# Kernel tuning notes

Measured on AMD Instinct MI355X. Metric: run time of the kernel, lower is better.

## Reference

```python
import jax, jax.numpy as jnp
import numpy as np

B, F, T, D, O = 8192, 512, 64, 6, 128
N_INTERNAL = 2 ** D - 1  # 63
N_LEAVES = 2 ** D        # 64


def smooth_step(t):
    tc = jnp.clip(t, -0.5, 0.5)
    return -2.0 * tc ** 3 + 1.5 * tc + 0.5


def setup_inputs() -> dict:
    key = jax.random.key(0)
    k1, k2, k3, k4 = jax.random.split(key, 4)
    x = jax.random.normal(k1, (B, F), dtype=jnp.float32)
    # Stacked per-node Linear weights in BFS (heap) order: node i -> row i.
    W_nodes = jax.random.normal(k2, (N_INTERNAL, F, T), dtype=jnp.float32) * (1.0 / np.sqrt(F))
    b_nodes = jax.random.normal(k3, (N_INTERNAL, T), dtype=jnp.float32) * 0.01
    # Per-leaf mixing weight [out_features, num_trees], leaves in BFS order.
    W_leaf = jax.random.normal(k4, (N_LEAVES, O, T), dtype=jnp.float32)
    return {"x": x, "W_nodes": W_nodes, "b_nodes": b_nodes, "W_leaf": W_leaf}


def reference(x, W_nodes, b_nodes, W_leaf):
    n_internal = W_nodes.shape[0]
    depth = int(np.log2(n_internal + 1))
    # All internal-node gates in one stacked GEMM: [B, n_internal, T]
    s = smooth_step(jnp.einsum('bf,nft->bnt', x, W_nodes) + b_nodes[None, :, :])
    b, _, t = s.shape
    prob = jnp.ones((b, 1, t), dtype=s.dtype)  # root prob
    start = 0
    for lvl in range(depth):
        width = 2 ** lvl
        s_l = s[:, start:start + width]  # [B, width, T], nodes at this level
        start += width
        # node local j -> children local 2j (left, prob*s) and 2j+1 (right, prob*(1-s))
        prob = jnp.stack([prob * s_l, prob * (1.0 - s_l)], axis=2).reshape(b, 2 * width, t)
    # prob: [B, n_leaves, T]; mix per-leaf, per-tree weights -> [B, O]
    out = jnp.einsum('blt,lot->bo', prob, W_leaf)
    return out
```

## Files before the change

kernel.cpp:

```cpp
#include <hip/hip_runtime.h>
#include <hip/hip_fp16.h>

#define BATCH 8192
#define FDIM  512
#define NTREE 64
#define NODES 63
#define ODIM  128
#define NJP   4096
#define K2    4096
#define TPG   8

typedef _Float16 f16;
typedef _Float16 f16x2 __attribute__((ext_vector_type(2)));
typedef _Float16 f16x4 __attribute__((ext_vector_type(4)));
typedef _Float16 f16x8 __attribute__((ext_vector_type(8)));
typedef float    f32x4 __attribute__((ext_vector_type(4)));

#define XH_OFF   0
#define XH_SZ    ((size_t)BATCH*FDIM*2)
#define WNH_OFF  (XH_OFF + XH_SZ)
#define WNH_SZ   ((size_t)NJP*FDIM*2)
#define WLT_OFF  (WNH_OFF + WNH_SZ)
#define WLT_SZ   ((size_t)ODIM*K2*2)
#define PS_OFF   (WLT_OFF + WLT_SZ)
#define PS_SZ    ((size_t)TPG*BATCH*ODIM*4)
#define WS_NEEDED (PS_OFF + PS_SZ)

__device__ __forceinline__ float smooth_step_f(float t) {
    float tc = fminf(fmaxf(t, -0.5f), 0.5f);
    return fmaf(tc, fmaf(-2.0f * tc, tc, 1.5f), 0.5f);
}

__device__ __forceinline__ void async16(const void* g, void* l) {
    __builtin_amdgcn_global_load_lds((__attribute__((address_space(1))) void*)g,
                                     (__attribute__((address_space(3))) void*)l,
                                     16, 0, 0);
}

__device__ __forceinline__ int sw_off(int row, int g) {
    return ((row >> 3) * 512) + (((row & 7) * 8 + (g ^ (row & 7))) * 8);
}

#define XBLK 4096
#define WLBLK 128
__global__ __launch_bounds__(256)
void prep_kernel(const float* __restrict__ x, const float* __restrict__ wn,
                 const float* __restrict__ wl,
                 f16* __restrict__ xh, f16* __restrict__ wnh, f16* __restrict__ wlt)
{
    __shared__ __align__(16) char smem[16640];
    const int bid = blockIdx.x;

    if (bid < XBLK) {
        size_t i = ((size_t)bid * 256 + threadIdx.x) * 4;
        float4 v = *(const float4*)(x + i);
        f16x4 o4 = { (f16)v.x, (f16)v.y, (f16)v.z, (f16)v.w };
        *(f16x4*)(xh + i) = o4;
        return;
    }
    if (bid < XBLK + WLBLK) {
        f16 (*tile)[72] = (f16(*)[72])smem;
        const int o    = bid - XBLK;
        const int lane = threadIdx.x & 63;
        const int w    = threadIdx.x >> 6;
        #pragma unroll
        for (int lc = 0; lc < 16; ++lc) {
            int l = w * 16 + lc;
            tile[lane][l] = (f16)wl[(size_t)l * (ODIM * NTREE) + o * 64 + lane];
        }
        __syncthreads();
        f16* orow = wlt + (size_t)o * K2;
        #pragma unroll
        for (int c = 0; c < 2; ++c) {
            int idx = (threadIdx.x * 2 + c) * 8;
            int t = idx >> 6, l = idx & 63;
            f16x8 v;
            #pragma unroll
            for (int e = 0; e < 8; ++e) v[e] = tile[t][l + e];
            *(f16x8*)(orow + idx) = v;
        }
        return;
    }
    {
        const int id   = bid - (XBLK + WLBLK);
        const int n    = id & 63;
        const int f0   = (id >> 6) * 64;
        const int lane = threadIdx.x & 63;
        const int w    = threadIdx.x >> 6;
        if (n == NODES) {
            #pragma unroll
            for (int tc = 0; tc < 16; ++tc) {
                int t = w * 16 + tc;
                wnh[(size_t)(t * 64 + NODES) * FDIM + f0 + lane] = (f16)0.0f;
            }
            return;
        }
        float (*tile)[65] = (float(*)[65])smem;
        const float* src = wn + (size_t)n * (FDIM * NTREE);
        #pragma unroll
        for (int i = 0; i < 16; ++i) {
            int fl = w * 16 + i;
            tile[fl][lane] = src[(size_t)(f0 + fl) * NTREE + lane];
        }
        __syncthreads();
        #pragma unroll
        for (int i = 0; i < 16; ++i) {
            int t = w * 16 + i;
            wnh[(size_t)(t * 64 + n) * FDIM + f0 + lane] = (f16)tile[lane][t];
        }
    }
}

__global__ __launch_bounds__(256, 2)
void fused_tree(const f16* __restrict__ xh, const f16* __restrict__ wnh,
                const float* __restrict__ bn, const f16* __restrict__ wlt,
                float* __restrict__ partial)
{
    __shared__ f16 SH[16640];
    const int tid  = threadIdx.x;
    const int lane = tid & 63;
    const int w    = tid >> 6;
    const int wm   = w & 1;
    const int wn   = w >> 1;
    const int row0 = blockIdx.x * 128;
    const int tpg  = blockIdx.y;

    const int lr = lane >> 3;
    const int lg = (lane & 7) ^ lr;
    const int frow = tid & 127;
    const int ftr  = tid >> 7;

    f32x4 lacc[4][4] = {};

    for (int tpi = 0; tpi < 4; ++tpi) {
        const int tp = tpg * 4 + tpi;
        const int j0 = tp * 128;

        f32x4 acc[4][4] = {};
        for (int k0 = 0; k0 < FDIM; k0 += 64) {
            #pragma unroll
            for (int q = 0; q < 8; ++q) {
                int id = w * 8 + q;
                if (id < 16) {
                    int r = id * 8 + lr;
                    async16(xh + (size_t)(row0 + r) * FDIM + k0 + lg * 8, &SH[id * 512 + lane * 8]);
                } else {
                    int c = id - 16;
                    int r = c * 8 + lr;
                    async16(wnh + (size_t)(j0 + r) * FDIM + k0 + lg * 8, &SH[8192 + c * 512 + lane * 8]);
                }
            }
            __syncthreads();
            #pragma unroll
            for (int ks = 0; ks < 2; ++ks) {
                int g = ks * 4 + (lane >> 4);
                f16x8 bfr[4];
                #pragma unroll
                for (int tn = 0; tn < 4; ++tn) {
                    int j = wn * 64 + tn * 16 + (lane & 15);
                    bfr[tn] = *(const f16x8*)&SH[8192 + sw_off(j, g)];
                }
                #pragma unroll
                for (int tm = 0; tm < 4; ++tm) {
                    int m = wm * 64 + tm * 16 + (lane & 15);
                    f16x8 afr = *(const f16x8*)&SH[sw_off(m, g)];
                    #pragma unroll
                    for (int tn = 0; tn < 4; ++tn)
                        acc[tm][tn] = __builtin_amdgcn_mfma_f32_16x16x32_f16(afr, bfr[tn], acc[tm][tn], 0, 0, 0);
                }
            }
            __syncthreads();
        }

        #pragma unroll
        for (int tn = 0; tn < 4; ++tn) {
            int col = wn * 64 + tn * 16 + (lane & 15);
            int nn  = col & 63;
            int tt  = (j0 + col) >> 6;
            float bias = (nn < NODES) ? bn[nn * NTREE + tt] : 0.0f;
            #pragma unroll
            for (int tm = 0; tm < 4; ++tm) {
                #pragma unroll
                for (int r = 0; r < 4; ++r) {
                    int row = wm * 64 + tm * 16 + (lane >> 4) * 4 + r;
                    SH[row * 130 + col] = (f16)smooth_step_f(acc[tm][tn][r] + bias);
                }
            }
        }
        __syncthreads();

        f16x8 ov[8];
        {
            const f16* gp = &SH[frow * 130 + ftr * 64];
            float g[64];
            #pragma unroll
            for (int c = 0; c < 32; ++c) {
                f16x2 v = *(const f16x2*)(gp + 2 * c);
                g[2 * c]     = (float)v[0];
                g[2 * c + 1] = (float)v[1];
            }
            float pr[32];
            pr[0] = 1.0f;
            int bse = 0;
            #pragma unroll
            for (int lvl = 0; lvl < 5; ++lvl) {
                const int width = 1 << lvl;
                #pragma unroll
                for (int i = width - 1; i >= 0; --i) {
                    float p = pr[i], s = g[bse + i];
                    pr[2 * i]     = p * s;
                    pr[2 * i + 1] = p * (1.0f - s);
                }
                bse += width;
            }
            #pragma unroll
            for (int i = 0; i < 32; ++i) {
                float s5 = g[31 + i];
                float p  = pr[i];
                ov[i >> 2][(i & 3) * 2]     = (f16)(p * s5);
                ov[i >> 2][(i & 3) * 2 + 1] = (f16)(p * (1.0f - s5));
            }
        }
        __syncthreads();

        #pragma unroll
        for (int h = 0; h < 2; ++h) {
            if (ftr == h) {
                #pragma unroll
                for (int g2 = 0; g2 < 8; ++g2)
                    *(f16x8*)&SH[sw_off(frow, g2)] = ov[g2];
            }
            #pragma unroll
            for (int q = 0; q < 4; ++q) {
                int c = w * 4 + q;
                int o = c * 8 + lr;
                async16(wlt + (size_t)o * K2 + j0 + h * 64 + lg * 8,
                        &SH[8192 + c * 512 + lane * 8]);
            }
            __syncthreads();

            #pragma unroll
            for (int ks = 0; ks < 2; ++ks) {
                int g = ks * 4 + (lane >> 4);
                f16x8 bfr[4];
                #pragma unroll
                for (int tn = 0; tn < 4; ++tn) {
                    int o = wn * 64 + tn * 16 + (lane & 15);
                    bfr[tn] = *(const f16x8*)&SH[8192 + sw_off(o, g)];
                }
                #pragma unroll
                for (int tm = 0; tm < 4; ++tm) {
                    int m = wm * 64 + tm * 16 + (lane & 15);
                    f16x8 afr = *(const f16x8*)&SH[sw_off(m, g)];
                    #pragma unroll
                    for (int tn = 0; tn < 4; ++tn)
                        lacc[tm][tn] = __builtin_amdgcn_mfma_f32_16x16x32_f16(afr, bfr[tn], lacc[tm][tn], 0, 0, 0);
                }
            }
            __syncthreads();
        }
    }

    float* dst = partial + (size_t)tpg * BATCH * ODIM;
    #pragma unroll
    for (int tn = 0; tn < 4; ++tn) {
        int o = wn * 64 + tn * 16 + (lane & 15);
        #pragma unroll
        for (int tm = 0; tm < 4; ++tm) {
            #pragma unroll
            for (int r = 0; r < 4; ++r) {
                int row = row0 + wm * 64 + tm * 16 + (lane >> 4) * 4 + r;
                dst[(size_t)row * ODIM + o] = lacc[tm][tn][r];
            }
        }
    }
}

__global__ void reduce_kernel(const float* __restrict__ partial, float* __restrict__ out) {
    size_t i = ((size_t)blockIdx.x * blockDim.x + threadIdx.x) * 4;
    f32x4 a = *(const f32x4*)(partial + i);
    #pragma unroll
    for (int k = 1; k < TPG; ++k)
        a += *(const f32x4*)(partial + (size_t)k * BATCH * ODIM + i);
    *(f32x4*)(out + i) = a;
}

#define ROWS 8
__global__ __launch_bounds__(256, 2)
void soft_tree_fallback(const float* __restrict__ x, const float* __restrict__ Wn,
                        const float* __restrict__ bn, const float* __restrict__ Wl,
                        float* __restrict__ out)
{
    __shared__ __half s_lds[ROWS][NODES][NTREE];
    const int lane = threadIdx.x & 63;
    const int w    = threadIdx.x >> 6;
    const long row0 = (long)blockIdx.x * ROWS;
    for (int n = w; n < NODES; n += 4) {
        const float* wp = Wn + ((long)n * FDIM) * NTREE + lane;
        const float* xp = x + row0 * FDIM;
        float acc[ROWS];
        #pragma unroll
        for (int r = 0; r < ROWS; ++r) acc[r] = 0.0f;
        #pragma unroll 8
        for (int f = 0; f < FDIM; ++f) {
            float wv = wp[(long)f * NTREE];
            #pragma unroll
            for (int r = 0; r < ROWS; ++r)
                acc[r] = fmaf(xp[r * FDIM + f], wv, acc[r]);
        }
        float bias = bn[n * NTREE + lane];
        #pragma unroll
        for (int r = 0; r < ROWS; ++r)
            s_lds[r][n][lane] = __float2half(smooth_step_f(acc[r] + bias));
    }
    __syncthreads();
    const int r0 = w * 2, r1 = w * 2 + 1;
    float pr0[64], pr1[64];
    {
        pr0[0] = 1.0f; pr1[0] = 1.0f;
        int base = 0;
        #pragma unroll
        for (int lvl = 0; lvl < 6; ++lvl) {
            const int width = 1 << lvl;
            #pragma unroll
            for (int i = width - 1; i >= 0; --i) {
                float sa = __half2float(s_lds[r0][base + i][lane]);
                float sb = __half2float(s_lds[r1][base + i][lane]);
                float pa = pr0[i], pb = pr1[i];
                pr0[2 * i] = pa * sa; pr0[2 * i + 1] = pa * (1.0f - sa);
                pr1[2 * i] = pb * sb; pr1[2 * i + 1] = pb * (1.0f - sb);
            }
            base += width;
        }
    }
    for (int o = 0; o < ODIM; ++o) {
        const float* wlp = Wl + (long)o * NTREE + lane;
        float c0 = 0.0f, c1 = 0.0f;
        #pragma unroll
        for (int l = 0; l < 64; ++l) {
            float wv = wlp[(long)l * (ODIM * NTREE)];
            c0 = fmaf(pr0[l], wv, c0);
            c1 = fmaf(pr1[l], wv, c1);
        }
        #pragma unroll
        for (int off = 32; off > 0; off >>= 1) {
            c0 += __shfl_xor(c0, off, 64);
            c1 += __shfl_xor(c1, off, 64);
        }
        if (lane == 0) {
            out[(row0 + r0) * ODIM + o] = c0;
            out[(row0 + r1) * ODIM + o] = c1;
        }
    }
}

extern "C" void kernel_launch(void* const* d_in, const int* in_sizes, int n_in,
                              void* d_out, int out_size, void* d_ws, size_t ws_size,
                              hipStream_t stream) {
    const float* x  = (const float*)d_in[0];
    const float* Wn = (const float*)d_in[1];
    const float* bn = (const float*)d_in[2];
    const float* Wl = (const float*)d_in[3];
    float* out = (float*)d_out;

    if (ws_size < WS_NEEDED) {
        soft_tree_fallback<<<BATCH / ROWS, 256, 0, stream>>>(x, Wn, bn, Wl, out);
        return;
    }

    f16*   xh  = (f16*)((char*)d_ws + XH_OFF);
    f16*   wnh = (f16*)((char*)d_ws + WNH_OFF);
    f16*   wlt = (f16*)((char*)d_ws + WLT_OFF);
    float* ps  = (float*)((char*)d_ws + PS_OFF);

    prep_kernel<<<XBLK + WLBLK + 512, 256, 0, stream>>>(x, Wn, Wl, xh, wnh, wlt);
    fused_tree<<<dim3(BATCH / 128, TPG), 256, 0, stream>>>(xh, wnh, bn, wlt, ps);
    reduce_kernel<<<(BATCH * ODIM) / (256 * 4), 256, 0, stream>>>(ps, out);
}
```

Measured before the change: 149.7 us.

## Double-buffer node GEMM tiles and prefetch leaf weights during gate epilogue

Doubles LDS so the next k-slice of x and node weights loads asynchronously while MFMAs run on the current slice, leaving one barrier per k-step. Both halves of the leaf weight tile are prefetched into a separate LDS region before the smooth-step and tree-probability epilogue, so that load overlaps the epilogue. Both probability halves are stored at once, and some barriers become lighter LDS-only waits. The cost is about twice the LDS per block, which may limit occupancy.

Result: no change. 151.9 us (+1.5%).

```diff
diff --git a/kernel.cpp b/kernel.cpp
--- a/kernel.cpp
+++ b/kernel.cpp
@@ -37,6 +37,12 @@
                                      16, 0, 0);
 }
 
+__device__ __forceinline__ void bar_lds() {
+    asm volatile("s_waitcnt lgkmcnt(0)" ::: "memory");
+    __builtin_amdgcn_s_barrier();
+    asm volatile("" ::: "memory");
+}
+
 __device__ __forceinline__ int sw_off(int row, int g) {
     return ((row >> 3) * 512) + (((row & 7) * 8 + (g ^ (row & 7))) * 8);
 }
@@ -111,12 +117,30 @@
     }
 }
 
+#define STAGE_NODE(dstbase, kk)                                                \
+    {                                                                          \
+        _Pragma("unroll")                                                      \
+        for (int q = 0; q < 8; ++q) {                                          \
+            int id = w * 8 + q;                                                \
+            if (id < 16) {                                                     \
+                int r = id * 8 + lr;                                           \
+                async16(xh + (size_t)(row0 + r) * FDIM + (kk) + lg * 8,        \
+                        &SH[(dstbase) + id * 512 + lane * 8]);                 \
+            } else {                                                           \
+                int c = id - 16;                                               \
+                int r = c * 8 + lr;                                            \
+                async16(wnh + (size_t)(j0 + r) * FDIM + (kk) + lg * 8,         \
+                        &SH[(dstbase) + 8192 + c * 512 + lane * 8]);           \
+            }                                                                  \
+        }                                                                      \
+    }
+
 __global__ __launch_bounds__(256, 2)
 void fused_tree(const f16* __restrict__ xh, const f16* __restrict__ wnh,
                 const float* __restrict__ bn, const f16* __restrict__ wlt,
                 float* __restrict__ partial)
 {
-    __shared__ f16 SH[16640];
+    __shared__ __align__(16) f16 SH[33024];
     const int tid  = threadIdx.x;
     const int lane = tid & 63;
     const int w    = tid >> 6;
@@ -137,20 +161,14 @@
         const int j0 = tp * 128;
 
         f32x4 acc[4][4] = {};
-        for (int k0 = 0; k0 < FDIM; k0 += 64) {
-            #pragma unroll
-            for (int q = 0; q < 8; ++q) {
-                int id = w * 8 + q;
-                if (id < 16) {
-                    int r = id * 8 + lr;
-                    async16(xh + (size_t)(row0 + r) * FDIM + k0 + lg * 8, &SH[id * 512 + lane * 8]);
-                } else {
-                    int c = id - 16;
-                    int r = c * 8 + lr;
-                    async16(wnh + (size_t)(j0 + r) * FDIM + k0 + lg * 8, &SH[8192 + c * 512 + lane * 8]);
-                }
-            }
-            __syncthreads();
+        STAGE_NODE(0, 0);
+        __syncthreads();
+
+        #pragma unroll 2
+        for (int t = 0; t < 8; ++t) {
+            const int base = (t & 1) * 16384;
+            if (t < 7)
+                STAGE_NODE(((t + 1) & 1) * 16384, (t + 1) * 64);
             #pragma unroll
             for (int ks = 0; ks < 2; ++ks) {
                 int g = ks * 4 + (lane >> 4);
@@ -158,18 +176,28 @@
                 #pragma unroll
                 for (int tn = 0; tn < 4; ++tn) {
                     int j = wn * 64 + tn * 16 + (lane & 15);
-                    bfr[tn] = *(const f16x8*)&SH[8192 + sw_off(j, g)];
+                    bfr[tn] = *(const f16x8*)&SH[base + 8192 + sw_off(j, g)];
                 }
                 #pragma unroll
                 for (int tm = 0; tm < 4; ++tm) {
                     int m = wm * 64 + tm * 16 + (lane & 15);
-                    f16x8 afr = *(const f16x8*)&SH[sw_off(m, g)];
+                    f16x8 afr = *(const f16x8*)&SH[base + sw_off(m, g)];
                     #pragma unroll
                     for (int tn = 0; tn < 4; ++tn)
                         acc[tm][tn] = __builtin_amdgcn_mfma_f32_16x16x32_f16(afr, bfr[tn], acc[tm][tn], 0, 0, 0);
                 }
             }
             __syncthreads();
+        }
+
+        #pragma unroll
+        for (int q = 0; q < 8; ++q) {
+            int id = w * 8 + q;
+            int h  = id >> 4;
+            int c  = id & 15;
+            int o  = c * 8 + lr;
+            async16(wlt + (size_t)o * K2 + j0 + h * 64 + lg * 8,
+                    &SH[16640 + h * 8192 + c * 512 + lane * 8]);
         }
 
         #pragma unroll
@@ -187,18 +215,19 @@
                 }
             }
         }
-        __syncthreads();
+        bar_lds();
 
         f16x8 ov[8];
         {
             const f16* gp = &SH[frow * 130 + ftr * 64];
-            float g[64];
+            float gg[64];
             #pragma unroll
             for (int c = 0; c < 32; ++c) {
                 f16x2 v = *(const f16x2*)(gp + 2 * c);
-                g[2 * c]     = (float)v[0];
-                g[2 * c + 1] = (float)v[1];
-            }
+                gg[2 * c]     = (float)v[0];
+                gg[2 * c + 1] = (float)v[1];
+            }
+            bar_lds();
             float pr[32];
             pr[0] = 1.0f;
             int bse = 0;
@@ -207,7 +236,7 @@
                 const int width = 1 << lvl;
                 #pragma unroll
                 for (int i = width - 1; i >= 0; --i) {
-                    float p = pr[i], s = g[bse + i];
+                    float p = pr[i], s = gg[bse + i];
                     pr[2 * i]     = p * s;
                     pr[2 * i + 1] = p * (1.0f - s);
                 }
@@ -215,30 +244,20 @@
             }
             #pragma unroll
             for (int i = 0; i < 32; ++i) {
-                float s5 = g[31 + i];
+                float s5 = gg[31 + i];
                 float p  = pr[i];
                 ov[i >> 2][(i & 3) * 2]     = (f16)(p * s5);
                 ov[i >> 2][(i & 3) * 2 + 1] = (f16)(p * (1.0f - s5));
             }
         }
+
+        #pragma unroll
+        for (int g2 = 0; g2 < 8; ++g2)
+            *(f16x8*)&SH[ftr * 8192 + sw_off(frow, g2)] = ov[g2];
         __syncthreads();
 
         #pragma unroll
         for (int h = 0; h < 2; ++h) {
-            if (ftr == h) {
-                #pragma unroll
-                for (int g2 = 0; g2 < 8; ++g2)
-                    *(f16x8*)&SH[sw_off(frow, g2)] = ov[g2];
-            }
-            #pragma unroll
-            for (int q = 0; q < 4; ++q) {
-                int c = w * 4 + q;
-                int o = c * 8 + lr;
-                async16(wlt + (size_t)o * K2 + j0 + h * 64 + lg * 8,
-                        &SH[8192 + c * 512 + lane * 8]);
-            }
-            __syncthreads();
-
             #pragma unroll
             for (int ks = 0; ks < 2; ++ks) {
                 int g = ks * 4 + (lane >> 4);
@@ -246,19 +265,19 @@
                 #pragma unroll
                 for (int tn = 0; tn < 4; ++tn) {
                     int o = wn * 64 + tn * 16 + (lane & 15);
-                    bfr[tn] = *(const f16x8*)&SH[8192 + sw_off(o, g)];
+                    bfr[tn] = *(const f16x8*)&SH[16640 + h * 8192 + sw_off(o, g)];
                 }
                 #pragma unroll
                 for (int tm = 0; tm < 4; ++tm) {
                     int m = wm * 64 + tm * 16 + (lane & 15);
-                    f16x8 afr = *(const f16x8*)&SH[sw_off(m, g)];
+                    f16x8 afr = *(const f16x8*)&SH[h * 8192 + sw_off(m, g)];
                     #pragma unroll
                     for (int tn = 0; tn < 4; ++tn)
                         lacc[tm][tn] = __builtin_amdgcn_mfma_f32_16x16x32_f16(afr, bfr[tn], lacc[tm][tn], 0, 0, 0);
                 }
             }
-            __syncthreads();
-        }
+        }
+        __syncthreads();
     }
 
     float* dst = partial + (size_t)tpg * BATCH * ODIM;
```

## Pre-pack operands in MFMA fragment order and load fragments directly from global

Applied to the files above, without the earlier changes.

The prep kernel now writes x, node weights and leaf weights as f16 tiles already laid out in MFMA fragment order. The fused kernel then reads A/B fragments straight from global memory into registers instead of staging them through LDS with async loads and barriers. Both halves of the leaf-probability tile are also written to LDS at once, which removes per-half barriers. The cost is that every wave now depends on global or L2 latency for each fragment with no LDS reuse across waves, and the prep kernel does strided, uncoalesced reads of the weights.

After: 161.8 us. +8.1%, slower.

```diff
diff --git a/kernel.cpp b/kernel.cpp
--- a/kernel.cpp
+++ b/kernel.cpp
@@ -31,104 +31,93 @@
     return fmaf(tc, fmaf(-2.0f * tc, tc, 1.5f), 0.5f);
 }
 
-__device__ __forceinline__ void async16(const void* g, void* l) {
-    __builtin_amdgcn_global_load_lds((__attribute__((address_space(1))) void*)g,
-                                     (__attribute__((address_space(3))) void*)l,
-                                     16, 0, 0);
-}
-
 __device__ __forceinline__ int sw_off(int row, int g) {
     return ((row >> 3) * 512) + (((row & 7) * 8 + (g ^ (row & 7))) * 8);
 }
 
-#define XBLK 4096
-#define WLBLK 128
 __global__ __launch_bounds__(256)
 void prep_kernel(const float* __restrict__ x, const float* __restrict__ wn,
                  const float* __restrict__ wl,
-                 f16* __restrict__ xh, f16* __restrict__ wnh, f16* __restrict__ wlt)
+                 f16* __restrict__ xf, f16* __restrict__ wnf, f16* __restrict__ wlf)
 {
-    __shared__ __align__(16) char smem[16640];
-    const int bid = blockIdx.x;
-
-    if (bid < XBLK) {
-        size_t i = ((size_t)bid * 256 + threadIdx.x) * 4;
-        float4 v = *(const float4*)(x + i);
-        f16x4 o4 = { (f16)v.x, (f16)v.y, (f16)v.z, (f16)v.w };
-        *(f16x4*)(xh + i) = o4;
-        return;
-    }
-    if (bid < XBLK + WLBLK) {
-        f16 (*tile)[72] = (f16(*)[72])smem;
-        const int o    = bid - XBLK;
-        const int lane = threadIdx.x & 63;
-        const int w    = threadIdx.x >> 6;
-        #pragma unroll
-        for (int lc = 0; lc < 16; ++lc) {
-            int l = w * 16 + lc;
-            tile[lane][l] = (f16)wl[(size_t)l * (ODIM * NTREE) + o * 64 + lane];
-        }
-        __syncthreads();
-        f16* orow = wlt + (size_t)o * K2;
-        #pragma unroll
-        for (int c = 0; c < 2; ++c) {
-            int idx = (threadIdx.x * 2 + c) * 8;
-            int t = idx >> 6, l = idx & 63;
+    const int bid = blockIdx.x, tid = threadIdx.x;
+    if (bid < 512) {
+        const int bx = bid >> 3, k0 = bid & 7;
+        f16* dst = xf + ((size_t)bx * 8192 + (size_t)k0 * 1024) * 8;
+        #pragma unroll
+        for (int c = 0; c < 4; ++c) {
+            int fid  = c * 256 + tid;
+            int lane = fid & 63, ks = (fid >> 6) & 1, tm = (fid >> 7) & 3, wm = (fid >> 9) & 1;
+            int row  = bx * 128 + wm * 64 + tm * 16 + (lane & 15);
+            int k    = k0 * 64 + (ks * 4 + (lane >> 4)) * 8;
+            const float* s = x + (size_t)row * FDIM + k;
+            float4 a = *(const float4*)s, b = *(const float4*)(s + 4);
+            f16x8 v = { (f16)a.x, (f16)a.y, (f16)a.z, (f16)a.w,
+                        (f16)b.x, (f16)b.y, (f16)b.z, (f16)b.w };
+            *(f16x8*)(dst + (size_t)fid * 8) = v;
+        }
+    } else if (bid < 768) {
+        const int id = bid - 512, tp = id >> 3, k0 = id & 7;
+        f16* dst = wnf + ((size_t)tp * 8192 + (size_t)k0 * 1024) * 8;
+        #pragma unroll
+        for (int c = 0; c < 4; ++c) {
+            int fid  = c * 256 + tid;
+            int lane = fid & 63, ks = (fid >> 6) & 1, tn = (fid >> 7) & 3, wq = (fid >> 9) & 1;
+            int col  = tp * 128 + wq * 64 + tn * 16 + (lane & 15);
+            int t    = col >> 6, n = col & 63;
+            int k    = k0 * 64 + (ks * 4 + (lane >> 4)) * 8;
             f16x8 v;
-            #pragma unroll
-            for (int e = 0; e < 8; ++e) v[e] = tile[t][l + e];
-            *(f16x8*)(orow + idx) = v;
-        }
-        return;
-    }
-    {
-        const int id   = bid - (XBLK + WLBLK);
-        const int n    = id & 63;
-        const int f0   = (id >> 6) * 64;
-        const int lane = threadIdx.x & 63;
-        const int w    = threadIdx.x >> 6;
-        if (n == NODES) {
-            #pragma unroll
-            for (int tc = 0; tc < 16; ++tc) {
-                int t = w * 16 + tc;
-                wnh[(size_t)(t * 64 + NODES) * FDIM + f0 + lane] = (f16)0.0f;
-            }
-            return;
-        }
-        float (*tile)[65] = (float(*)[65])smem;
-        const float* src = wn + (size_t)n * (FDIM * NTREE);
-        #pragma unroll
-        for (int i = 0; i < 16; ++i) {
-            int fl = w * 16 + i;
-            tile[fl][lane] = src[(size_t)(f0 + fl) * NTREE + lane];
-        }
-        __syncthreads();
-        #pragma unroll
-        for (int i = 0; i < 16; ++i) {
-            int t = w * 16 + i;
-            wnh[(size_t)(t * 64 + n) * FDIM + f0 + lane] = (f16)tile[lane][t];
+            if (n == NODES) {
+                #pragma unroll
+                for (int e = 0; e < 8; ++e) v[e] = (f16)0.0f;
+            } else {
+                const float* s = wn + ((size_t)n * FDIM + k) * NTREE + t;
+                #pragma unroll
+                for (int e = 0; e < 8; ++e) v[e] = (f16)s[(size_t)e * NTREE];
+            }
+            *(f16x8*)(dst + (size_t)fid * 8) = v;
+        }
+    } else {
+        const int tp = bid - 768;
+        f16* dst = wlf + (size_t)tp * 2048 * 8;
+        #pragma unroll
+        for (int c = 0; c < 8; ++c) {
+            int fid  = c * 256 + tid;
+            int lane = fid & 63, ks = (fid >> 6) & 1, tn = (fid >> 7) & 3, wq = (fid >> 9) & 1;
+            int h    = (fid >> 10) & 1;
+            int o    = wq * 64 + tn * 16 + (lane & 15);
+            int t    = tp * 2 + h;
+            int l0   = (ks * 4 + (lane >> 4)) * 8;
+            const float* s = wl + ((size_t)l0 * ODIM + o) * NTREE + t;
+            f16x8 v;
+            #pragma unroll
+            for (int e = 0; e < 8; ++e) v[e] = (f16)s[(size_t)e * ODIM * NTREE];
+            *(f16x8*)(dst + (size_t)fid * 8) = v;
         }
     }
 }
 
 __global__ __launch_bounds__(256, 2)
-void fused_tree(const f16* __restrict__ xh, const f16* __restrict__ wnh,
-                const float* __restrict__ bn, const f16* __restrict__ wlt,
+void fused_tree(const f16* __restrict__ xhF, const f16* __restrict__ wnhF,
+                const float* __restrict__ bn, const f16* __restrict__ wltF,
                 float* __restrict__ partial)
 {
-    __shared__ f16 SH[16640];
+    __shared__ __align__(16) f16 SH[16640];
     const int tid  = threadIdx.x;
     const int lane = tid & 63;
     const int w    = tid >> 6;
     const int wm   = w & 1;
-    const int wn   = w >> 1;
+    const int wq   = w >> 1;
     const int row0 = blockIdx.x * 128;
     const int tpg  = blockIdx.y;
 
-    const int lr = lane >> 3;
-    const int lg = (lane & 7) ^ lr;
     const int frow = tid & 127;
     const int ftr  = tid >> 7;
+
+    const f16x8* __restrict__ xv = (const f16x8*)xhF;
+    const f16x8* __restrict__ wv = (const f16x8*)wnhF;
+    const f16x8* __restrict__ lv = (const f16x8*)wltF;
+    const size_t xb = (size_t)blockIdx.x * 8192 + (size_t)wm * 512 + lane;
 
     f32x4 lacc[4][4] = {};
 
@@ -136,45 +125,29 @@
         const int tp = tpg * 4 + tpi;
         const int j0 = tp * 128;
 
+        const size_t wb = (size_t)tp * 8192 + (size_t)wq * 512 + lane;
         f32x4 acc[4][4] = {};
-        for (int k0 = 0; k0 < FDIM; k0 += 64) {
-            #pragma unroll
-            for (int q = 0; q < 8; ++q) {
-                int id = w * 8 + q;
-                if (id < 16) {
-                    int r = id * 8 + lr;
-                    async16(xh + (size_t)(row0 + r) * FDIM + k0 + lg * 8, &SH[id * 512 + lane * 8]);
-                } else {
-                    int c = id - 16;
-                    int r = c * 8 + lr;
-                    async16(wnh + (size_t)(j0 + r) * FDIM + k0 + lg * 8, &SH[8192 + c * 512 + lane * 8]);
-                }
-            }
-            __syncthreads();
+        #pragma unroll 2
+        for (int k0 = 0; k0 < 8; ++k0) {
             #pragma unroll
             for (int ks = 0; ks < 2; ++ks) {
-                int g = ks * 4 + (lane >> 4);
                 f16x8 bfr[4];
                 #pragma unroll
-                for (int tn = 0; tn < 4; ++tn) {
-                    int j = wn * 64 + tn * 16 + (lane & 15);
-                    bfr[tn] = *(const f16x8*)&SH[8192 + sw_off(j, g)];
-                }
+                for (int tn = 0; tn < 4; ++tn)
+                    bfr[tn] = wv[wb + k0 * 1024 + tn * 128 + ks * 64];
                 #pragma unroll
                 for (int tm = 0; tm < 4; ++tm) {
-                    int m = wm * 64 + tm * 16 + (lane & 15);
-                    f16x8 afr = *(const f16x8*)&SH[sw_off(m, g)];
+                    f16x8 afr = xv[xb + k0 * 1024 + tm * 128 + ks * 64];
                     #pragma unroll
                     for (int tn = 0; tn < 4; ++tn)
                         acc[tm][tn] = __builtin_amdgcn_mfma_f32_16x16x32_f16(afr, bfr[tn], acc[tm][tn], 0, 0, 0);
                 }
             }
-            __syncthreads();
         }
 
         #pragma unroll
         for (int tn = 0; tn < 4; ++tn) {
-            int col = wn * 64 + tn * 16 + (lane & 15);
+            int col = wq * 64 + tn * 16 + (lane & 15);
             int nn  = col & 63;
             int tt  = (j0 + col) >> 6;
             float bias = (nn < NODES) ? bn[nn * NTREE + tt] : 0.0f;
@@ -192,13 +165,14 @@
         f16x8 ov[8];
         {
             const f16* gp = &SH[frow * 130 + ftr * 64];
-            float g[64];
+            float gg[64];
             #pragma unroll
             for (int c = 0; c < 32; ++c) {
                 f16x2 v = *(const f16x2*)(gp + 2 * c);
-                g[2 * c]     = (float)v[0];
-                g[2 * c + 1] = (float)v[1];
-            }
+                gg[2 * c]     = (float)v[0];
+                gg[2 * c + 1] = (float)v[1];
+            }
+            __syncthreads();
             float pr[32];
             pr[0] = 1.0f;
             int bse = 0;
@@ -207,7 +181,7 @@
                 const int width = 1 << lvl;
                 #pragma unroll
                 for (int i = width - 1; i >= 0; --i) {
-                    float p = pr[i], s = g[bse + i];
+                    float p = pr[i], s = gg[bse + i];
                     pr[2 * i]     = p * s;
                     pr[2 * i + 1] = p * (1.0f - s);
                 }
@@ -215,56 +189,45 @@
             }
             #pragma unroll
             for (int i = 0; i < 32; ++i) {
-                float s5 = g[31 + i];
+                float s5 = gg[31 + i];
                 float p  = pr[i];
                 ov[i >> 2][(i & 3) * 2]     = (f16)(p * s5);
                 ov[i >> 2][(i & 3) * 2 + 1] = (f16)(p * (1.0f - s5));
             }
         }
+
+        #pragma unroll
+        for (int g2 = 0; g2 < 8; ++g2)
+            *(f16x8*)&SH[ftr * 8192 + sw_off(frow, g2)] = ov[g2];
         __syncthreads();
 
+        const size_t lb = (size_t)tp * 2048 + (size_t)wq * 512 + lane;
         #pragma unroll
         for (int h = 0; h < 2; ++h) {
-            if (ftr == h) {
-                #pragma unroll
-                for (int g2 = 0; g2 < 8; ++g2)
-                    *(f16x8*)&SH[sw_off(frow, g2)] = ov[g2];
-            }
-            #pragma unroll
-            for (int q = 0; q < 4; ++q) {
-                int c = w * 4 + q;
-                int o = c * 8 + lr;
-                async16(wlt + (size_t)o * K2 + j0 + h * 64 + lg * 8,
-                        &SH[8192 + c * 512 + lane * 8]);
-            }
-            __syncthreads();
-
             #pragma unroll
             for (int ks = 0; ks < 2; ++ks) {
                 int g = ks * 4 + (lane >> 4);
                 f16x8 bfr[4];
                 #pragma unroll
-                for (int tn = 0; tn < 4; ++tn) {
-                    int o = wn * 64 + tn * 16 + (lane & 15);
-                    bfr[tn] = *(const f16x8*)&SH[8192 + sw_off(o, g)];
-                }
+                for (int tn = 0; tn < 4; ++tn)
+                    bfr[tn] = lv[lb + h * 1024 + tn * 128 + ks * 64];
                 #pragma unroll
                 for (int tm = 0; tm < 4; ++tm) {
                     int m = wm * 64 + tm * 16 + (lane & 15);
-                    f16x8 afr = *(const f16x8*)&SH[sw_off(m, g)];
+                    f16x8 afr = *(const f16x8*)&SH[h * 8192 + sw_off(m, g)];
                     #pragma unroll
                     for (int tn = 0; tn < 4; ++tn)
                         lacc[tm][tn] = __builtin_amdgcn_mfma_f32_16x16x32_f16(afr, bfr[tn], lacc[tm][tn], 0, 0, 0);
                 }
             }
-            __syncthreads();
-        }
+        }
+        __syncthreads();
     }
 
     float* dst = partial + (size_t)tpg * BATCH * ODIM;
     #pragma unroll
     for (int tn = 0; tn < 4; ++tn) {
-        int o = wn * 64 + tn * 16 + (lane & 15);
+        int o = wq * 64 + tn * 16 + (lane & 15);
         #pragma unroll
         for (int tm = 0; tm < 4; ++tm) {
             #pragma unroll
@@ -373,7 +336,7 @@
     f16*   wlt = (f16*)((char*)d_ws + WLT_OFF);
     float* ps  = (float*)((char*)d_ws + PS_OFF);
 
-    prep_kernel<<<XBLK + WLBLK + 512, 256, 0, stream>>>(x, Wn, Wl, xh, wnh, wlt);
+    prep_kernel<<<800, 256, 0, stream>>>(x, Wn, Wl, xh, wnh, wlt);
     fused_tree<<<dim3(BATCH / 128, TPG), 256, 0, stream>>>(xh, wnh, bn, wlt, ps);
     reduce_kernel<<<(BATCH * ODIM) / (256 * 4), 256, 0, stream>>>(ps, out);
 }
```
